# Kernel optimization log

Hardware: AMD Instinct MI355X
Metric: run time of the kernel (lower is better)

Reference implementation:

```python
import jax, jax.numpy as jnp
import numpy as np

NUM_CLASSES = 80
NUM_TOP_QUERIES = 300


def setup_inputs() -> dict:
    key = jax.random.key(0)
    k1, k2 = jax.random.split(key)
    logits = jax.random.normal(k1, (256, 1000, 80), dtype=jnp.float32)
    boxes = jax.random.uniform(k2, (256, 1000, 4), dtype=jnp.float32)  # cxcywh in (0,1)
    return {"logits": logits, "boxes": boxes}


def _cxcywh_to_xyxy(b):
    cx, cy, w, h = b[..., 0], b[..., 1], b[..., 2], b[..., 3]
    return jnp.stack([cx - 0.5 * w, cy - 0.5 * h, cx + 0.5 * w, cy + 0.5 * h], axis=-1)


def reference(logits, boxes):
    B = logits.shape[0]
    bbox_pred = _cxcywh_to_xyxy(boxes)                      # [B,Q,4]
    scores_all = jax.nn.sigmoid(logits).reshape(B, -1)      # [B,Q*C]
    scores, index = jax.lax.top_k(scores_all, NUM_TOP_QUERIES)  # [B,K]
    labels = index % NUM_CLASSES                            # class id
    qidx = index // NUM_CLASSES                             # query id
    boxes_out = jnp.take_along_axis(bbox_pred, qidx[..., None], axis=1)  # [B,K,4]
    return labels, boxes_out, scores
```

## Files before the change

kernel.cpp:

```cpp
#include <hip/hip_runtime.h>
#include <math.h>

typedef unsigned long long u64;
typedef unsigned int u32;

#define NB 256
#define NQ 1000
#define NC 80
#define QC 80000
#define TOPK 300
#define CAP 2048
#define NTHREADS 1024

__global__ __launch_bounds__(NTHREADS) void postproc_kernel(
    const float* __restrict__ logits,
    const float4* __restrict__ boxes,
    float* __restrict__ out) {
  const int row = blockIdx.x;
  const int tid = threadIdx.x;

  __shared__ u64 s_keys[CAP];
  __shared__ int s_cnt;

  const float4* lp = (const float4*)logits + (size_t)row * (QC / 4);

  float T = 2.0f;
  int cnt = 0;
  for (int attempt = 0; attempt < 24; ++attempt) {
    __syncthreads();
    if (tid == 0) s_cnt = 0;
    __syncthreads();
    for (int i = tid; i < QC / 4; i += NTHREADS) {
      float4 v = lp[i];
      float xs[4] = {v.x, v.y, v.z, v.w};
#pragma unroll
      for (int c = 0; c < 4; ++c) {
        float x = xs[c];
        if (x > T) {
          int pos = atomicAdd(&s_cnt, 1);
          if (pos < CAP) {
            u32 bits = __float_as_uint(x);
            u32 idx = (u32)(4 * i + c);
            s_keys[pos] = ((u64)bits << 32) | (u64)(0xFFFFFFFFu - idx);
          }
        }
      }
    }
    __syncthreads();
    cnt = s_cnt;
    if (cnt >= TOPK && cnt <= CAP) break;
    T = (cnt < TOPK) ? (T - 0.9f) : (T + 0.45f);
  }
  if (cnt > CAP) cnt = CAP;

  for (int i = cnt + tid; i < CAP; i += NTHREADS) s_keys[i] = 0ull;
  __syncthreads();

  for (int size = 2; size <= CAP; size <<= 1) {
    for (int stride = size >> 1; stride > 0; stride >>= 1) {
      int i = tid;
      int lo = 2 * i - (i & (stride - 1));
      int hi = lo + stride;
      u64 a = s_keys[lo];
      u64 b = s_keys[hi];
      bool desc = (lo & size) == 0;
      bool sw = desc ? (a < b) : (a > b);
      if (sw) {
        s_keys[lo] = b;
        s_keys[hi] = a;
      }
      __syncthreads();
    }
  }

  if (tid < TOPK) {
    const int k = tid;
    float* labels_out = out;
    float* boxes_out = out + NB * TOPK;
    float* scores_out = out + NB * TOPK * 5;

    float lab = 0.0f, score = 0.0f;
    float4 bo = make_float4(0.0f, 0.0f, 0.0f, 0.0f);
    if (k < cnt) {
      u64 key = s_keys[k];
      u32 idx = 0xFFFFFFFFu - (u32)(key & 0xFFFFFFFFull);
      float x = __uint_as_float((u32)(key >> 32));
      int q = (int)(idx / NC);
      int c = (int)(idx - (u32)q * NC);
      lab = (float)c;
      score = (float)(1.0 / (1.0 + exp(-(double)x)));
      float4 bb = boxes[(size_t)row * NQ + q];
      float hw = 0.5f * bb.z, hh = 0.5f * bb.w;
      bo.x = bb.x - hw;
      bo.y = bb.y - hh;
      bo.z = bb.x + hw;
      bo.w = bb.y + hh;
    }
    labels_out[row * TOPK + k] = lab;
    scores_out[row * TOPK + k] = score;
    ((float4*)boxes_out)[row * TOPK + k] = bo;
  }
}

extern "C" void kernel_launch(void* const* d_in, const int* in_sizes, int n_in,
                              void* d_out, int out_size, void* d_ws, size_t ws_size,
                              hipStream_t stream) {
  const float* logits = (const float*)d_in[0];
  const float4* boxes = (const float4*)d_in[1];
  float* out = (float*)d_out;
  postproc_kernel<<<NB, NTHREADS, 0, stream>>>(logits, boxes, out);
}
```

Before: 134.3 us.

## Split candidate collection across segment blocks before per-row sort

```diff
diff --git a/kernel.cpp b/kernel.cpp
--- a/kernel.cpp
+++ b/kernel.cpp
@@ -10,11 +10,68 @@
 #define QC 80000
 #define TOPK 300
 #define CAP 2048
-#define NTHREADS 1024
+#define SEGS 8
+#define SEGQ (QC / 4 / SEGS)
+#define CAPB 512
+#define CTHREADS 256
+#define STHREADS 1024
 
-__global__ __launch_bounds__(NTHREADS) void postproc_kernel(
-    const float* __restrict__ logits,
-    const float4* __restrict__ boxes,
+#define WS_BUF_OFF 4096
+
+
+__global__ __launch_bounds__(CTHREADS) void collect_kernel(
+    const float* __restrict__ logits, u32* __restrict__ ctr,
+    u64* __restrict__ cand) {
+  const int row = blockIdx.x >> 3;
+  const int seg = blockIdx.x & 7;
+  const int tid = threadIdx.x;
+
+  __shared__ u64 s_buf[CAPB];
+  __shared__ int s_cnt;
+  __shared__ int s_base;
+
+  if (tid == 0) s_cnt = 0;
+  __syncthreads();
+
+  const float4* lp = (const float4*)logits + (size_t)row * (QC / 4);
+  const float T = 2.0f;
+  const int i0 = seg * SEGQ;
+
+  for (int i = i0 + tid; i < i0 + SEGQ; i += CTHREADS) {
+    float4 v = lp[i];
+    float xs[4] = {v.x, v.y, v.z, v.w};
+#pragma unroll
+    for (int c = 0; c < 4; ++c) {
+      float x = xs[c];
+      if (x > T) {
+        int pos = atomicAdd(&s_cnt, 1);
+        if (pos < CAPB) {
+          u32 idx = (u32)(4 * i + c);
+          s_buf[pos] = ((u64)__float_as_uint(x) << 32) | (u64)(0xFFFFFFFFu - idx);
+        }
+      }
+    }
+  }
+  __syncthreads();
+
+  if (tid == 0) {
+    int n = s_cnt;
+    s_base = (int)atomicAdd(&ctr[row], (u32)n);
+    if (n > CAPB) atomicAdd(&ctr[row], 1u << 20);
+  }
+  __syncthreads();
+
+  int n = min(s_cnt, CAPB);
+  u64* rowbuf = cand + (size_t)row * CAP;
+  for (int j = tid; j < n; j += CTHREADS) {
+    int dst = s_base + j;
+    if (dst < CAP) rowbuf[dst] = s_buf[j];
+  }
+}
+
+__global__ __launch_bounds__(STHREADS) void sort_emit_kernel(
+    const float* __restrict__ logits, const float4* __restrict__ boxes,
+    const u32* __restrict__ ctr, const u64* __restrict__ cand,
     float* __restrict__ out) {
   const int row = blockIdx.x;
   const int tid = threadIdx.x;
@@ -22,38 +79,42 @@
   __shared__ u64 s_keys[CAP];
   __shared__ int s_cnt;
 
-  const float4* lp = (const float4*)logits + (size_t)row * (QC / 4);
+  int cnt = (int)ctr[row];
 
-  float T = 2.0f;
-  int cnt = 0;
-  for (int attempt = 0; attempt < 24; ++attempt) {
-    __syncthreads();
-    if (tid == 0) s_cnt = 0;
-    __syncthreads();
-    for (int i = tid; i < QC / 4; i += NTHREADS) {
-      float4 v = lp[i];
-      float xs[4] = {v.x, v.y, v.z, v.w};
+  if (cnt >= TOPK && cnt <= CAP) {
+    const u64* rowbuf = cand + (size_t)row * CAP;
+    for (int i = tid; i < cnt; i += STHREADS) s_keys[i] = rowbuf[i];
+  } else {
+    const float4* lp = (const float4*)logits + (size_t)row * (QC / 4);
+    float T = 2.0f;
+    for (int attempt = 0; attempt < 24; ++attempt) {
+      __syncthreads();
+      if (tid == 0) s_cnt = 0;
+      __syncthreads();
+      for (int i = tid; i < QC / 4; i += STHREADS) {
+        float4 v = lp[i];
+        float xs[4] = {v.x, v.y, v.z, v.w};
 #pragma unroll
-      for (int c = 0; c < 4; ++c) {
-        float x = xs[c];
-        if (x > T) {
-          int pos = atomicAdd(&s_cnt, 1);
-          if (pos < CAP) {
-            u32 bits = __float_as_uint(x);
-            u32 idx = (u32)(4 * i + c);
-            s_keys[pos] = ((u64)bits << 32) | (u64)(0xFFFFFFFFu - idx);
+        for (int c = 0; c < 4; ++c) {
+          float x = xs[c];
+          if (x > T) {
+            int pos = atomicAdd(&s_cnt, 1);
+            if (pos < CAP) {
+              u32 idx = (u32)(4 * i + c);
+              s_keys[pos] = ((u64)__float_as_uint(x) << 32) | (u64)(0xFFFFFFFFu - idx);
+            }
           }
         }
       }
+      __syncthreads();
+      cnt = s_cnt;
+      if (cnt >= TOPK && cnt <= CAP) break;
+      T = (cnt < TOPK) ? (T - 0.9f) : (T + 0.45f);
     }
-    __syncthreads();
-    cnt = s_cnt;
-    if (cnt >= TOPK && cnt <= CAP) break;
-    T = (cnt < TOPK) ? (T - 0.9f) : (T + 0.45f);
+    if (cnt > CAP) cnt = CAP;
   }
-  if (cnt > CAP) cnt = CAP;
 
-  for (int i = cnt + tid; i < CAP; i += NTHREADS) s_keys[i] = 0ull;
+  for (int i = cnt + tid; i < CAP; i += STHREADS) s_keys[i] = 0ull;
   __syncthreads();
 
   for (int size = 2; size <= CAP; size <<= 1) {
@@ -64,8 +125,7 @@
       u64 a = s_keys[lo];
       u64 b = s_keys[hi];
       bool desc = (lo & size) == 0;
-      bool sw = desc ? (a < b) : (a > b);
-      if (sw) {
+      if (desc ? (a < b) : (a > b)) {
         s_keys[lo] = b;
         s_keys[hi] = a;
       }
@@ -108,5 +168,11 @@
   const float* logits = (const float*)d_in[0];
   const float4* boxes = (const float4*)d_in[1];
   float* out = (float*)d_out;
-  postproc_kernel<<<NB, NTHREADS, 0, stream>>>(logits, boxes, out);
+
+  u32* ctr = (u32*)d_ws;
+  u64* cand = (u64*)((char*)d_ws + WS_BUF_OFF);
+
+  hipMemsetAsync(ctr, 0, NB * sizeof(u32), stream);
+  collect_kernel<<<NB * SEGS, CTHREADS, 0, stream>>>(logits, ctr, cand);
+  sort_emit_kernel<<<NB, STHREADS, 0, stream>>>(logits, boxes, ctr, cand, out);
 }
```

New measurement: 140.0 us. +4.2%, slower.

## Tune threshold bisection, shrink candidate buffer, use register/shuffle bitonic sort

Applied to the files above, without the earlier changes.

```diff
diff --git a/kernel.cpp b/kernel.cpp
--- a/kernel.cpp
+++ b/kernel.cpp
@@ -8,9 +8,18 @@
 #define NQ 1000
 #define NC 80
 #define QC 80000
+#define NQ4 (QC / 4)
 #define TOPK 300
-#define CAP 2048
+#define CAP 512
 #define NTHREADS 1024
+
+#define T_INIT 2.585f
+
+__device__ __forceinline__ u64 shfl_xor_u64(u64 v, int mask) {
+  int lo = __shfl_xor((int)(u32)(v & 0xFFFFFFFFull), mask, 64);
+  int hi = __shfl_xor((int)(u32)(v >> 32), mask, 64);
+  return ((u64)(u32)hi << 32) | (u64)(u32)lo;
+}
 
 __global__ __launch_bounds__(NTHREADS) void postproc_kernel(
     const float* __restrict__ logits,
@@ -22,67 +31,92 @@
   __shared__ u64 s_keys[CAP];
   __shared__ int s_cnt;
 
-  const float4* lp = (const float4*)logits + (size_t)row * (QC / 4);
+  const float4* lp = (const float4*)logits + (size_t)row * NQ4;
 
-  float T = 2.0f;
+  float T = T_INIT;
+  float tlo = -1.0f, thi = 7.0f;
   int cnt = 0;
+
+  auto filt = [&](float x, u32 idx) {
+    if (x > T) {
+      int pos = atomicAdd(&s_cnt, 1);
+      if (pos < CAP)
+        s_keys[pos] = ((u64)__float_as_uint(x) << 32) | (u64)(0xFFFFFFFFu - idx);
+    }
+  };
+
   for (int attempt = 0; attempt < 24; ++attempt) {
     __syncthreads();
     if (tid == 0) s_cnt = 0;
     __syncthreads();
-    for (int i = tid; i < QC / 4; i += NTHREADS) {
+
+    for (int i = tid; i < 16384; i += 4 * NTHREADS) {
+      float4 v0 = lp[i];
+      float4 v1 = lp[i + NTHREADS];
+      float4 v2 = lp[i + 2 * NTHREADS];
+      float4 v3 = lp[i + 3 * NTHREADS];
+      filt(v0.x, 4 * i);                  filt(v0.y, 4 * i + 1);
+      filt(v0.z, 4 * i + 2);              filt(v0.w, 4 * i + 3);
+      int i1 = i + NTHREADS;
+      filt(v1.x, 4 * i1);                 filt(v1.y, 4 * i1 + 1);
+      filt(v1.z, 4 * i1 + 2);             filt(v1.w, 4 * i1 + 3);
+      int i2 = i + 2 * NTHREADS;
+      filt(v2.x, 4 * i2);                 filt(v2.y, 4 * i2 + 1);
+      filt(v2.z, 4 * i2 + 2);             filt(v2.w, 4 * i2 + 3);
+      int i3 = i + 3 * NTHREADS;
+      filt(v3.x, 4 * i3);                 filt(v3.y, 4 * i3 + 1);
+      filt(v3.z, 4 * i3 + 2);             filt(v3.w, 4 * i3 + 3);
+    }
+    for (int i = 16384 + tid; i < NQ4; i += NTHREADS) {
       float4 v = lp[i];
-      float xs[4] = {v.x, v.y, v.z, v.w};
-#pragma unroll
-      for (int c = 0; c < 4; ++c) {
-        float x = xs[c];
-        if (x > T) {
-          int pos = atomicAdd(&s_cnt, 1);
-          if (pos < CAP) {
-            u32 bits = __float_as_uint(x);
-            u32 idx = (u32)(4 * i + c);
-            s_keys[pos] = ((u64)bits << 32) | (u64)(0xFFFFFFFFu - idx);
-          }
-        }
-      }
+      filt(v.x, 4 * i);  filt(v.y, 4 * i + 1);
+      filt(v.z, 4 * i + 2);  filt(v.w, 4 * i + 3);
     }
+
     __syncthreads();
     cnt = s_cnt;
     if (cnt >= TOPK && cnt <= CAP) break;
-    T = (cnt < TOPK) ? (T - 0.9f) : (T + 0.45f);
+    if (cnt < TOPK) thi = T; else tlo = T;
+    T = 0.5f * (tlo + thi);
   }
   if (cnt > CAP) cnt = CAP;
 
-  for (int i = cnt + tid; i < CAP; i += NTHREADS) s_keys[i] = 0ull;
-  __syncthreads();
+  u64 key = 0;
+  if (tid < CAP && tid < cnt) key = s_keys[tid];
 
-  for (int size = 2; size <= CAP; size <<= 1) {
-    for (int stride = size >> 1; stride > 0; stride >>= 1) {
-      int i = tid;
-      int lo = 2 * i - (i & (stride - 1));
-      int hi = lo + stride;
-      u64 a = s_keys[lo];
-      u64 b = s_keys[hi];
-      bool desc = (lo & size) == 0;
-      bool sw = desc ? (a < b) : (a > b);
-      if (sw) {
-        s_keys[lo] = b;
-        s_keys[hi] = a;
+  for (int k = 2; k <= CAP; k <<= 1) {
+    for (int j = k >> 1; j > 0; j >>= 1) {
+      if (j >= 64) {
+        __syncthreads();
+        if (tid < CAP) s_keys[tid] = key;
+        __syncthreads();
+        if (tid < CAP) {
+          u64 other = s_keys[tid ^ j];
+          bool iLower = (tid & j) == 0;
+          bool dirAsc = (tid & k) != 0;
+          bool keepMin = (dirAsc == iLower);
+          key = keepMin ? (key < other ? key : other)
+                        : (key > other ? key : other);
+        }
+      } else if (tid < CAP) {
+        u64 other = shfl_xor_u64(key, j);
+        bool iLower = (tid & j) == 0;
+        bool dirAsc = (tid & k) != 0;
+        bool keepMin = (dirAsc == iLower);
+        key = keepMin ? (key < other ? key : other)
+                      : (key > other ? key : other);
       }
-      __syncthreads();
     }
   }
 
   if (tid < TOPK) {
-    const int k = tid;
     float* labels_out = out;
     float* boxes_out = out + NB * TOPK;
     float* scores_out = out + NB * TOPK * 5;
 
     float lab = 0.0f, score = 0.0f;
     float4 bo = make_float4(0.0f, 0.0f, 0.0f, 0.0f);
-    if (k < cnt) {
-      u64 key = s_keys[k];
+    if (tid < cnt) {
       u32 idx = 0xFFFFFFFFu - (u32)(key & 0xFFFFFFFFull);
       float x = __uint_as_float((u32)(key >> 32));
       int q = (int)(idx / NC);
@@ -96,9 +130,9 @@
       bo.z = bb.x + hw;
       bo.w = bb.y + hh;
     }
-    labels_out[row * TOPK + k] = lab;
-    scores_out[row * TOPK + k] = score;
-    ((float4*)boxes_out)[row * TOPK + k] = bo;
+    labels_out[row * TOPK + tid] = lab;
+    scores_out[row * TOPK + tid] = score;
+    ((float4*)boxes_out)[row * TOPK + tid] = bo;
   }
 }
 
```

Result: faster. 123.0 us (median of 2 runs) (-8.4%).
